# Kernel tuning notes

Measured on AMD Instinct MI355X. Metric: run time of the kernel, lower is better.

The kernel has to match this reference:

```python
import jax, jax.numpy as jnp
import numpy as np

B_SZ, L, H, P, G, N, CS = 2, 2048, 32, 64, 1, 128, 256


def _i8(k, shape):
    return jax.random.randint(k, shape, -127, 128, dtype=jnp.int32).astype(jnp.int8)


def setup_inputs() -> dict:
    key = jax.random.key(0)
    k = jax.random.split(key, 7)
    return {
        "x": _i8(k[0], (B_SZ, L, H, P)),          # quantized int8 activations
        "dt": _i8(k[1], (B_SZ, L, H)),
        "B": _i8(k[2], (B_SZ, L, G, N)),
        "C": _i8(k[3], (B_SZ, L, G, N)),
        "q_A_log": _i8(k[4], (H,)),               # int8 quantized A_log
        "q_D": _i8(k[5], (H,)),                   # int8 quantized D (D_has_hdim=False)
        "dt_bias": jax.random.normal(k[6], (H,), jnp.float32) * 0.1,
        "A_log_scale": jnp.float32(0.02),
        "D_scale": jnp.float32(0.01),
        "dt_scale": jnp.float32(0.03),
        "x_scale": jnp.float32(0.05),
        "B_scale": jnp.float32(0.05),
        "C_scale": jnp.float32(0.05),
    }


def _chunk_scan(x, dt, B, C, q_A_log, q_D, dt_bias,
                A_log_scale, D_scale, dt_scale, x_scale, B_scale, C_scale):
    f32 = jnp.float32
    b, l, h, p = x.shape
    g, n = B.shape[2], B.shape[3]
    cs = CS
    nc = l // cs

    # --- inline dequantization (per-tensor scales, nhead/ndim groups == 0) ---
    xf = x.astype(f32) * x_scale                       # (b, l, h, p)
    dtf = jax.nn.softplus(dt.astype(f32) * dt_scale + dt_bias)   # (b, l, h), dt_limit=(0, inf)
    A = -jnp.exp(q_A_log.astype(f32) * A_log_scale)    # (h,)
    Bf = B.astype(f32) * B_scale                       # (b, l, g, n)
    Cf = C.astype(f32) * C_scale

    # --- chunk the sequence ---
    xc = xf.reshape(b, nc, cs, h, p)
    dtc = dtf.reshape(b, nc, cs, h)
    Bc = Bf.reshape(b, nc, cs, g, n)
    Cc = Cf.reshape(b, nc, cs, g, n)
    rep = h // g
    Bh = jnp.repeat(Bc, rep, axis=3)                   # (b, nc, cs, h, n)
    Ch = jnp.repeat(Cc, rep, axis=3)

    dA = dtc * A                                       # (b, nc, cs, h), <= 0
    cum = jnp.cumsum(dA, axis=2)                       # cumulative log-decay within chunk

    # --- per-chunk states: sum_s exp(cum[-1]-cum[s]) * dt[s] * B[s] (x) x[s] ---
    decay_states = jnp.exp(cum[:, :, -1:, :] - cum)    # (b, nc, cs, h)
    states = jnp.einsum('bzlhn,bzlh,bzlhp->bzhpn', Bh, dtc * decay_states, xc)

    # --- inter-chunk recurrence (sequential scan over chunks) ---
    chunk_decay = jnp.exp(cum[:, :, -1, :])            # (b, nc, h)

    def step(carry, inp):
        s_c, d_c = inp                                 # (b, h, p, n), (b, h)
        new = d_c[:, :, None, None] * carry + s_c
        return new, carry                              # emit state entering this chunk

    states_t = jnp.moveaxis(states, 1, 0)              # (nc, b, h, p, n)
    decay_t = jnp.moveaxis(chunk_decay, 1, 0)          # (nc, b, h)
    final_state, prev_states = jax.lax.scan(
        step, jnp.zeros((b, h, p, n), f32), (states_t, decay_t))
    prev_states = jnp.moveaxis(prev_states, 0, 1)      # (b, nc, h, p, n)

    # --- inter-chunk output: C[l] . state_in * exp(cum[l]) ---
    y_inter = jnp.einsum('bzlhn,bzhpn,bzlh->bzlhp', Ch, prev_states, jnp.exp(cum))

    # --- intra-chunk output: causal (C.B) attention with decay weights ---
    cumT = jnp.moveaxis(cum, 3, 2)                     # (b, nc, h, cs)
    diff = cumT[..., :, None] - cumT[..., None, :]     # (b, nc, h, cs, cs): cum[l]-cum[s]
    mask = jnp.tril(jnp.ones((cs, cs), bool))
    decay_m = jnp.exp(jnp.where(mask, diff, -jnp.inf)) # zero above diagonal, no overflow
    scores = (jnp.einsum('bzlhn,bzshn->bzhls', Ch, Bh)
              * decay_m
              * jnp.moveaxis(dtc, 3, 2)[..., None, :])
    y_intra = jnp.einsum('bzhls,bzshp->bzlhp', scores, xc)

    # --- skip connection D * x (per-head D) ---
    Df = q_D.astype(f32) * D_scale                     # (h,)
    y = (y_intra + y_inter).reshape(b, l, h, p) + xf * Df[None, None, :, None]
    return y


def reference(x, dt, B, C, q_A_log, q_D, dt_bias,
              A_log_scale, D_scale, dt_scale, x_scale, B_scale, C_scale):
    return _chunk_scan(x, dt, B, C, q_A_log, q_D, dt_bias,
                       A_log_scale, D_scale, dt_scale, x_scale, B_scale, C_scale)
```

## Files before the change

kernel.cpp:

```cpp
#include <hip/hip_runtime.h>
#include <math.h>

#define BB 2
#define LSEQ 2048
#define H 32
#define PDIM 64
#define NDIM 128
#define CS 256
#define NC 8

typedef _Float16 half8 __attribute__((ext_vector_type(8)));
typedef _Float16 half4 __attribute__((ext_vector_type(4)));
typedef float floatx4 __attribute__((ext_vector_type(4)));


__device__ __forceinline__ int dot4i8(int a, int b, int c) {
#if __has_builtin(__builtin_amdgcn_sdot4)
    return __builtin_amdgcn_sdot4(a, b, c, false);
#else
    c += ((a << 24) >> 24) * ((b << 24) >> 24);
    c += ((a << 16) >> 24) * ((b << 16) >> 24);
    c += ((a << 8) >> 24) * ((b << 8) >> 24);
    c += (a >> 24) * (b >> 24);
    return c;
#endif
}

__global__ __launch_bounds__(256) void kA(
    const int* __restrict__ Bm, const int* __restrict__ Cm,
    const float* __restrict__ Bs_p, const float* __restrict__ Cs_p,
    float* __restrict__ CBt, _Float16* __restrict__ Bt16T, _Float16* __restrict__ C16T)
{
    __shared__ int Bi[64][33];
    __shared__ int Ci[64][33];
    int t = threadIdx.x;
    int r = blockIdx.x % 26;
    int zz = blockIdx.x / 26;
    int z = zz & 7, b = zz >> 3;
    int bz = b * NC + z;
    if (r < 10) {
        const int LT[10] = {0,1,1,2,2,2,3,3,3,3};
        const int ST[10] = {0,0,1,0,1,2,0,1,2,3};
        int l0 = LT[r] * 64, s0 = ST[r] * 64;
        const int* Bp = Bm + (size_t)(b * LSEQ + z * CS + s0) * NDIM;
        const int* Cp = Cm + (size_t)(b * LSEQ + z * CS + l0) * NDIM;
        for (int i = t; i < 64 * 32; i += 256) {
            int rr = i >> 5, k = i & 31;
            const int* sb = Bp + rr * NDIM + k * 4;
            const int* sc = Cp + rr * NDIM + k * 4;
            Bi[rr][k] = (sb[0] & 255) | ((sb[1] & 255) << 8) | ((sb[2] & 255) << 16) | ((sb[3] & 255) << 24);
            Ci[rr][k] = (sc[0] & 255) | ((sc[1] & 255) << 8) | ((sc[2] & 255) << 16) | ((sc[3] & 255) << 24);
        }
        __syncthreads();
        float cbscale = (*Bs_p) * (*Cs_p);
        int ll = t & 63, lg = t >> 6;
        int acc[16];
#pragma unroll
        for (int i = 0; i < 16; ++i) acc[i] = 0;
        for (int k = 0; k < 32; ++k) {
            int cw = Ci[ll][k];
#pragma unroll
            for (int si = 0; si < 16; ++si)
                acc[si] = dot4i8(cw, Bi[lg * 16 + si][k], acc[si]);
        }
        int l = l0 + ll;
        int l16 = l >> 4, lm = l & 15;
        int sb8 = (s0 + lg * 16) >> 3;
        float* bp = CBt + ((size_t)(bz * 16 + l16) * 32 + sb8) * 128 + lm * 8;
#pragma unroll
        for (int g = 0; g < 2; ++g) {
            floatx4 v0, v1;
#pragma unroll
            for (int i = 0; i < 4; ++i) {
                v0[i] = (float)acc[g * 8 + i] * cbscale;
                v1[i] = (float)acc[g * 8 + 4 + i] * cbscale;
            }
            *(floatx4*)(bp + g * 128) = v0;
            *(floatx4*)(bp + g * 128 + 4) = v1;
        }
    } else {
        int slice = r - 10;
        {
            int lm = t >> 4, n8 = t & 15;
            const int* cp = Cm + (size_t)(b * LSEQ + z * CS + slice * 16 + lm) * NDIM + n8 * 8;
            int4 c0 = *(const int4*)cp;
            int4 c1 = *(const int4*)(cp + 4);
            half8 v;
            v[0] = (_Float16)(float)c0.x; v[1] = (_Float16)(float)c0.y;
            v[2] = (_Float16)(float)c0.z; v[3] = (_Float16)(float)c0.w;
            v[4] = (_Float16)(float)c1.x; v[5] = (_Float16)(float)c1.y;
            v[6] = (_Float16)(float)c1.z; v[7] = (_Float16)(float)c1.w;
            *(half8*)(C16T + ((size_t)(bz * 16 + slice) * 16 + n8) * 128 + lm * 8) = v;
        }
        {
            int nm = t & 15, s8l = t >> 4;
            int n16 = slice & 7, s8 = (slice >> 3) * 16 + s8l;
            const int* bp = Bm + (size_t)(b * LSEQ + z * CS + s8 * 8) * NDIM + n16 * 16 + nm;
            half8 v;
#pragma unroll
            for (int j = 0; j < 8; ++j) v[j] = (_Float16)(float)bp[(size_t)j * NDIM];
            *(half8*)(Bt16T + ((size_t)(bz * 8 + n16) * 32 + s8) * 128 + nm * 8) = v;
        }
    }
}

#define XC_PITCH 132
__global__ __launch_bounds__(256) void k013(
    const int* __restrict__ dt, const int* __restrict__ qA, const float* __restrict__ dt_bias,
    const float* __restrict__ A_scale_p, const float* __restrict__ dt_scale_p,
    const int* __restrict__ xq, const float* __restrict__ xs_p, const float* __restrict__ Bs_p,
    const _Float16* __restrict__ Bt16T,
    float* __restrict__ cum, float* __restrict__ cdecay,
    _Float16* __restrict__ xTdtT, signed char* __restrict__ x8,
    float* __restrict__ states)
{
    __shared__ float cumS[CS];
    __shared__ float cA[CS], cB[CS];
    __shared__ float wsum[4];
    __shared__ _Float16 xcS[2 * 32 * XC_PITCH];
    int t = threadIdx.x;
    int half = blockIdx.x & 1;
    int h = (blockIdx.x >> 1) & 31, z = (blockIdx.x >> 6) & 7, b = blockIdx.x >> 9;
    int bz = b * NC + z, bzh = bz * H + h;
    int lane6 = t & 63, w = t >> 6;

    float A = -__expf((float)qA[h] * (*A_scale_p));
    float raw = (float)dt[(size_t)(b * LSEQ + z * CS + t) * H + h];
    float xin = raw * (*dt_scale_p) + dt_bias[h];
    float sp = (xin > 20.f) ? xin : log1pf(__expf(xin));
    float v = sp * A;
#pragma unroll
    for (int off = 1; off < 64; off <<= 1) {
        float u = __shfl_up(v, off, 64);
        if (lane6 >= off) v += u;
    }
    if (lane6 == 63) wsum[w] = v;
    __syncthreads();
    float add = 0.f;
    for (int wv = 0; wv < w; ++wv) add += wsum[wv];
    float cumv = v + add;
    float cl = wsum[0] + wsum[1] + wsum[2] + wsum[3];
    float xs = *xs_p;
    if (half == 0) {
        cum[bzh * CS + t] = cumv;
        if (t == 0) cdecay[bzh] = __expf(cl);
    }
    cumS[t] = cumv;
    cA[t] = sp * xs;
    cB[t] = sp * __expf(cl - cumv) * xs * (*Bs_p);
    __syncthreads();

    int s8 = t & 31, pq = t >> 5;
    const int* xb = xq + ((size_t)(b * LSEQ + z * CS) * H + h) * PDIM + half * 32 + pq * 4;
    signed char* x8b = x8 + ((size_t)(b * LSEQ + z * CS) * H + h) * PDIM + half * 32 + pq * 4;
    {
        half8 va[4], vc[4];
#pragma unroll
        for (int j = 0; j < 8; ++j) {
            int s = s8 * 8 + j;
            int4 w4 = *(const int4*)(xb + (size_t)s * (H * PDIM));
            float a = cA[s], c = cB[s];
            signed char pk[4];
#define CVT(PL, V) { float xv = (float)(V); va[PL][j] = (_Float16)(xv * a); vc[PL][j] = (_Float16)(xv * c); pk[PL] = (signed char)(V); }
            CVT(0, w4.x) CVT(1, w4.y) CVT(2, w4.z) CVT(3, w4.w)
#undef CVT
            *(int*)pk;
            *(int*)(x8b + (size_t)s * (H * PDIM)) = *(int*)pk;
        }
#pragma unroll
        for (int pl = 0; pl < 4; ++pl) {
            int ploc = pq * 4 + pl;
            int p16l = ploc >> 4, pm = ploc & 15;
            *(half8*)(xTdtT + ((size_t)(bzh * 4 + half * 2 + p16l) * 32 + s8) * 128 + pm * 8) = va[pl];
            *(half8*)(xcS + (p16l * 32 + s8) * XC_PITCH + pm * 8) = vc[pl];
        }
    }
    __syncthreads();

    int m = lane6 & 15, q = lane6 >> 4;
    int p16l = w & 1, ntb = (w >> 1) * 4;
    const _Float16* abase = xcS + (p16l * 32) * XC_PITCH + m * 8;
    const _Float16* bbase = Bt16T + ((size_t)(bz * 8 + ntb) * 32) * 128 + m * 8;
    floatx4 acc[4] = {};
    for (int kk = 0; kk < 8; ++kk) {
        if (cl - cumS[kk * 32 + 31] < -30.f) continue;
        int s8k = kk * 4 + q;
        half8 a = *(const half8*)(abase + s8k * XC_PITCH);
#pragma unroll
        for (int i = 0; i < 4; ++i) {
            half8 bf = *(const half8*)(bbase + ((size_t)i * 32 + s8k) * 128);
            acc[i] = __builtin_amdgcn_mfma_f32_16x16x32_f16(a, bf, acc[i], 0, 0, 0);
        }
    }
    int p16 = half * 2 + p16l;
    float* sb = states + (size_t)bzh * (PDIM * NDIM);
#pragma unroll
    for (int i = 0; i < 4; ++i)
#pragma unroll
        for (int rr = 0; rr < 4; ++rr)
            sb[(size_t)(p16 * 16 + q * 4 + rr) * NDIM + (ntb + i) * 16 + m] = acc[i][rr];
}

__global__ __launch_bounds__(256) void k4_scan(
    const float* __restrict__ cdecay, const float* __restrict__ states,
    _Float16* __restrict__ statesHT)
{
    int idx = blockIdx.x * 256 + threadIdx.x;
    int n4 = (idx & 31) * 4, p = (idx >> 5) & 63, h = (idx >> 11) & 31, b = idx >> 16;
    int soff = p * 128 + n4;
    int toff = ((p >> 4) * 16 + (n4 >> 3)) * 128 + (p & 15) * 8 + (n4 & 7);
    floatx4 carry = {};
    for (int z = 0; z < NC; ++z) {
        int bzh = (b * NC + z) * H + h;
        floatx4 v = *(const floatx4*)(states + (size_t)bzh * 8192 + soff);
        float d = cdecay[bzh];
        half4 o;
#pragma unroll
        for (int i = 0; i < 4; ++i) o[i] = (_Float16)(carry[i] * 0.0625f);
        *(half4*)(statesHT + (size_t)bzh * 8192 + toff) = o;
#pragma unroll
        for (int i = 0; i < 4; ++i) carry[i] = d * carry[i] + v[i];
    }
}

__global__ __launch_bounds__(256) void k56(
    const signed char* __restrict__ x8, const int* __restrict__ qD,
    const float* __restrict__ cum, const float* __restrict__ CBt,
    const _Float16* __restrict__ xTdtT, const _Float16* __restrict__ C16T,
    const _Float16* __restrict__ statesHT,
    const float* __restrict__ Cs_p, const float* __restrict__ xs_p, const float* __restrict__ Ds_p,
    float* __restrict__ out)
{
    __shared__ float cumL[CS];
    __shared__ float ep[128][65];
    int t = threadIdx.x;
    int parity = blockIdx.x & 1;
    int h = (blockIdx.x >> 1) & 31, z = (blockIdx.x >> 6) & 7, b = blockIdx.x >> 9;
    int bz = b * NC + z, bzh = bz * H + h;
    cumL[t] = cum[bzh * CS + t];
    __syncthreads();
    int w = t >> 6, lane = t & 63, m = lane & 15, q = lane >> 4;
    int l16a[2] = {parity + 2 * w, parity + 2 * (7 - w)};
    floatx4 acc[2][4] = {};

    const _Float16* shb = statesHT + (size_t)bzh * 8192 + m * 8;
    const _Float16* cbase = C16T + (size_t)bz * 16 * 16 * 128 + m * 8;
    bool interact[2];
#pragma unroll
    for (int j = 0; j < 2; ++j) interact[j] = (cumL[l16a[j] * 16] > -80.f);
    for (int kk = 0; kk < 4; ++kk) {
        int n8 = kk * 4 + q;
        half8 bf[4];
#pragma unroll
        for (int pt = 0; pt < 4; ++pt)
            bf[pt] = *(const half8*)(shb + (pt * 16 + n8) * 128);
#pragma unroll
        for (int j = 0; j < 2; ++j) {
            if (!interact[j]) continue;
            half8 ha = *(const half8*)(cbase + ((size_t)l16a[j] * 16 + n8) * 128);
#pragma unroll
            for (int pt = 0; pt < 4; ++pt)
                acc[j][pt] = __builtin_amdgcn_mfma_f32_16x16x32_f16(ha, bf[pt], acc[j][pt], 0, 0, 0);
        }
    }
    float Cs16 = (*Cs_p) * 16.0f;
#pragma unroll
    for (int j = 0; j < 2; ++j)
#pragma unroll
        for (int r = 0; r < 4; ++r) {
            float e = __expf(cumL[l16a[j] * 16 + q * 4 + r]) * Cs16;
#pragma unroll
            for (int pt = 0; pt < 4; ++pt) acc[j][pt][r] *= e;
        }

    const float* cbtb = CBt + (size_t)bz * 16 * 32 * 128 + m * 8;
    const _Float16* xb = xTdtT + (size_t)bzh * 4 * 32 * 128 + m * 8;
    for (int kk = 0; kk < 8; ++kk) {
        bool ex[2];
#pragma unroll
        for (int j = 0; j < 2; ++j)
            ex[j] = (2 * kk <= l16a[j]) && (cumL[l16a[j] * 16] - cumL[kk * 32 + 31] >= -30.f);
        if (!ex[0] && !ex[1]) continue;
        int s8 = kk * 4 + q;
        half8 bf[4];
#pragma unroll
        for (int pt = 0; pt < 4; ++pt)
            bf[pt] = *(const half8*)(xb + ((size_t)pt * 32 + s8) * 128);
#pragma unroll
        for (int j = 0; j < 2; ++j) {
            if (!ex[j]) continue;
            int l16 = l16a[j];
            int lA = l16 * 16 + m;
            float cum_l = cumL[lA];
            const float* cp = cbtb + ((size_t)l16 * 32 + s8) * 128;
            floatx4 c0 = *(const floatx4*)cp;
            floatx4 c1 = *(const floatx4*)(cp + 4);
            half8 a;
#pragma unroll
            for (int jj = 0; jj < 8; ++jj) {
                int s = kk * 32 + q * 8 + jj;
                float cb = (jj < 4) ? c0[jj] : c1[jj - 4];
                float wv = cb * __expf(cum_l - cumL[s]);
                a[jj] = (_Float16)((s <= lA) ? wv : 0.f);
            }
#pragma unroll
            for (int pt = 0; pt < 4; ++pt)
                acc[j][pt] = __builtin_amdgcn_mfma_f32_16x16x32_f16(a, bf[pt], acc[j][pt], 0, 0, 0);
        }
    }

    float xsDf = (*xs_p) * ((float)qD[h] * (*Ds_p));
    __syncthreads();
#pragma unroll
    for (int j = 0; j < 2; ++j) {
        int kidx = (j == 0) ? w : 7 - w;
        int lbase = kidx * 16 + q * 4;
#pragma unroll
        for (int r = 0; r < 4; ++r)
#pragma unroll
            for (int pt = 0; pt < 4; ++pt)
                ep[lbase + r][pt * 16 + m] = acc[j][pt][r];
    }
    __syncthreads();
    int lloc = t >> 1;
    int kidx = lloc >> 4, row = lloc & 15;
    int l = (parity + 2 * kidx) * 16 + row;
    size_t go = ((size_t)(b * LSEQ + z * CS + l) * H + h) * PDIM + (t & 1) * 32;
    const float* er = &ep[lloc][(t & 1) * 32];
    const signed char* xp8 = x8 + go;
#pragma unroll
    for (int it = 0; it < 8; ++it) {
        int xw = *(const int*)(xp8 + it * 4);
        floatx4 vv;
        vv[0] = er[it * 4 + 0] + (float)((xw << 24) >> 24) * xsDf;
        vv[1] = er[it * 4 + 1] + (float)((xw << 16) >> 24) * xsDf;
        vv[2] = er[it * 4 + 2] + (float)((xw << 8) >> 24) * xsDf;
        vv[3] = er[it * 4 + 3] + (float)(xw >> 24) * xsDf;
        *(floatx4*)(out + go + it * 4) = vv;
    }
}

extern "C" void kernel_launch(void* const* d_in, const int* in_sizes, int n_in,
                              void* d_out, int out_size, void* d_ws, size_t ws_size,
                              hipStream_t stream)
{
    const int* xq = (const int*)d_in[0];
    const int* dt = (const int*)d_in[1];
    const int* Bm = (const int*)d_in[2];
    const int* Cm = (const int*)d_in[3];
    const int* qA = (const int*)d_in[4];
    const int* qD = (const int*)d_in[5];
    const float* dt_bias = (const float*)d_in[6];
    const float* A_scale = (const float*)d_in[7];
    const float* D_scale = (const float*)d_in[8];
    const float* dt_scale = (const float*)d_in[9];
    const float* x_scale = (const float*)d_in[10];
    const float* B_scale = (const float*)d_in[11];
    const float* C_scale = (const float*)d_in[12];
    float* out = (float*)d_out;

    char* ws = (char*)d_ws;
    float* cum          = (float*)(ws);
    float* cdecay       = (float*)(ws + 524288);
    float* CBt          = (float*)(ws + 526336);
    float* states       = (float*)(ws + 4720640);
    _Float16* xTdtT     = (_Float16*)(ws + 21497856);
    _Float16* statesHT  = (_Float16*)(ws + 38275072);
    _Float16* Bt16T     = (_Float16*)(ws + 46663680);
    _Float16* C16T      = (_Float16*)(ws + 47712256);
    signed char* x8     = (signed char*)(ws + 48760832);

    kA<<<dim3(416), dim3(256), 0, stream>>>(Bm, Cm, B_scale, C_scale, CBt, Bt16T, C16T);
    k013<<<dim3(1024), dim3(256), 0, stream>>>(dt, qA, dt_bias, A_scale, dt_scale,
                                               xq, x_scale, B_scale, Bt16T,
                                               cum, cdecay, xTdtT, x8, states);
    k4_scan<<<dim3(512), dim3(256), 0, stream>>>(cdecay, states, statesHT);
    k56<<<dim3(1024), dim3(256), 0, stream>>>(x8, qD, cum, CBt, xTdtT, C16T, statesHT,
                                              C_scale, x_scale, D_scale, out);
}
```

Baseline: 169.3 us.

## Store CB and chunk states in fp16 and split k56 blocks by P-half

```diff
diff --git a/kernel.cpp b/kernel.cpp
--- a/kernel.cpp
+++ b/kernel.cpp
@@ -29,7 +29,7 @@
 __global__ __launch_bounds__(256) void kA(
     const int* __restrict__ Bm, const int* __restrict__ Cm,
     const float* __restrict__ Bs_p, const float* __restrict__ Cs_p,
-    float* __restrict__ CBt, _Float16* __restrict__ Bt16T, _Float16* __restrict__ C16T)
+    _Float16* __restrict__ CBh, _Float16* __restrict__ Bt16T, _Float16* __restrict__ C16T)
 {
     __shared__ int Bi[64][33];
     __shared__ int Ci[64][33];
@@ -66,17 +66,13 @@
         int l = l0 + ll;
         int l16 = l >> 4, lm = l & 15;
         int sb8 = (s0 + lg * 16) >> 3;
-        float* bp = CBt + ((size_t)(bz * 16 + l16) * 32 + sb8) * 128 + lm * 8;
+        _Float16* bp = CBh + ((size_t)(bz * 16 + l16) * 32 + sb8) * 128 + lm * 8;
 #pragma unroll
         for (int g = 0; g < 2; ++g) {
-            floatx4 v0, v1;
-#pragma unroll
-            for (int i = 0; i < 4; ++i) {
-                v0[i] = (float)acc[g * 8 + i] * cbscale;
-                v1[i] = (float)acc[g * 8 + 4 + i] * cbscale;
-            }
-            *(floatx4*)(bp + g * 128) = v0;
-            *(floatx4*)(bp + g * 128 + 4) = v1;
+            half8 v;
+#pragma unroll
+            for (int i = 0; i < 8; ++i) v[i] = (_Float16)((float)acc[g * 8 + i] * cbscale);
+            *(half8*)(bp + g * 128) = v;
         }
     } else {
         int slice = r - 10;
@@ -112,7 +108,7 @@
     const _Float16* __restrict__ Bt16T,
     float* __restrict__ cum, float* __restrict__ cdecay,
     _Float16* __restrict__ xTdtT, signed char* __restrict__ x8,
-    float* __restrict__ states)
+    _Float16* __restrict__ statesF16)
 {
     __shared__ float cumS[CS];
     __shared__ float cA[CS], cB[CS];
@@ -142,7 +138,7 @@
     float cl = wsum[0] + wsum[1] + wsum[2] + wsum[3];
     float xs = *xs_p;
     if (half == 0) {
-        cum[bzh * CS + t] = cumv;
+        cum[(size_t)bzh * CS + t] = cumv;
         if (t == 0) cdecay[bzh] = __expf(cl);
     }
     cumS[t] = cumv;
@@ -164,7 +160,6 @@
 #define CVT(PL, V) { float xv = (float)(V); va[PL][j] = (_Float16)(xv * a); vc[PL][j] = (_Float16)(xv * c); pk[PL] = (signed char)(V); }
             CVT(0, w4.x) CVT(1, w4.y) CVT(2, w4.z) CVT(3, w4.w)
 #undef CVT
-            *(int*)pk;
             *(int*)(x8b + (size_t)s * (H * PDIM)) = *(int*)pk;
         }
 #pragma unroll
@@ -193,118 +188,113 @@
         }
     }
     int p16 = half * 2 + p16l;
-    float* sb = states + (size_t)bzh * (PDIM * NDIM);
+    _Float16* sb = statesF16 + (size_t)bzh * 8192;
 #pragma unroll
     for (int i = 0; i < 4; ++i)
 #pragma unroll
         for (int rr = 0; rr < 4; ++rr)
-            sb[(size_t)(p16 * 16 + q * 4 + rr) * NDIM + (ntb + i) * 16 + m] = acc[i][rr];
+            sb[(size_t)(p16 * 16 + (ntb + i) * 2 + (m >> 3)) * 128 + (q * 4 + rr) * 8 + (m & 7)] =
+                (_Float16)(acc[i][rr] * 0.0625f);
 }
 
 __global__ __launch_bounds__(256) void k4_scan(
-    const float* __restrict__ cdecay, const float* __restrict__ states,
+    const float* __restrict__ cdecay, const _Float16* __restrict__ statesF16,
     _Float16* __restrict__ statesHT)
 {
     int idx = blockIdx.x * 256 + threadIdx.x;
-    int n4 = (idx & 31) * 4, p = (idx >> 5) & 63, h = (idx >> 11) & 31, b = idx >> 16;
-    int soff = p * 128 + n4;
-    int toff = ((p >> 4) * 16 + (n4 >> 3)) * 128 + (p & 15) * 8 + (n4 & 7);
+    int off4 = (idx & 2047) * 4;
+    int h = (idx >> 11) & 31, b = idx >> 16;
     floatx4 carry = {};
     for (int z = 0; z < NC; ++z) {
         int bzh = (b * NC + z) * H + h;
-        floatx4 v = *(const floatx4*)(states + (size_t)bzh * 8192 + soff);
+        half4 v4 = *(const half4*)(statesF16 + (size_t)bzh * 8192 + off4);
         float d = cdecay[bzh];
         half4 o;
 #pragma unroll
-        for (int i = 0; i < 4; ++i) o[i] = (_Float16)(carry[i] * 0.0625f);
-        *(half4*)(statesHT + (size_t)bzh * 8192 + toff) = o;
-#pragma unroll
-        for (int i = 0; i < 4; ++i) carry[i] = d * carry[i] + v[i];
+        for (int i = 0; i < 4; ++i) o[i] = (_Float16)carry[i];
+        *(half4*)(statesHT + (size_t)bzh * 8192 + off4) = o;
+#pragma unroll
+        for (int i = 0; i < 4; ++i) carry[i] = d * carry[i] + (float)v4[i];
     }
 }
 
 __global__ __launch_bounds__(256) void k56(
     const signed char* __restrict__ x8, const int* __restrict__ qD,
-    const float* __restrict__ cum, const float* __restrict__ CBt,
+    const float* __restrict__ cum, const _Float16* __restrict__ CBh,
     const _Float16* __restrict__ xTdtT, const _Float16* __restrict__ C16T,
     const _Float16* __restrict__ statesHT,
     const float* __restrict__ Cs_p, const float* __restrict__ xs_p, const float* __restrict__ Ds_p,
     float* __restrict__ out)
 {
     __shared__ float cumL[CS];
-    __shared__ float ep[128][65];
+    __shared__ float ep[128][33];
     int t = threadIdx.x;
-    int parity = blockIdx.x & 1;
+    int ph = blockIdx.x & 1;
     int h = (blockIdx.x >> 1) & 31, z = (blockIdx.x >> 6) & 7, b = blockIdx.x >> 9;
     int bz = b * NC + z, bzh = bz * H + h;
-    cumL[t] = cum[bzh * CS + t];
+    cumL[t] = cum[(size_t)bzh * CS + t];
     __syncthreads();
     int w = t >> 6, lane = t & 63, m = lane & 15, q = lane >> 4;
-    int l16a[2] = {parity + 2 * w, parity + 2 * (7 - w)};
-    floatx4 acc[2][4] = {};
+    floatx4 acc[4][2] = {};
 
     const _Float16* shb = statesHT + (size_t)bzh * 8192 + m * 8;
     const _Float16* cbase = C16T + (size_t)bz * 16 * 16 * 128 + m * 8;
-    bool interact[2];
-#pragma unroll
-    for (int j = 0; j < 2; ++j) interact[j] = (cumL[l16a[j] * 16] > -80.f);
+    bool interact[4];
+#pragma unroll
+    for (int j = 0; j < 4; ++j) interact[j] = (cumL[(4 * j + w) * 16] > -80.f);
     for (int kk = 0; kk < 4; ++kk) {
         int n8 = kk * 4 + q;
-        half8 bf[4];
-#pragma unroll
-        for (int pt = 0; pt < 4; ++pt)
-            bf[pt] = *(const half8*)(shb + (pt * 16 + n8) * 128);
-#pragma unroll
-        for (int j = 0; j < 2; ++j) {
+        half8 bf[2];
+#pragma unroll
+        for (int pt = 0; pt < 2; ++pt)
+            bf[pt] = *(const half8*)(shb + ((ph * 2 + pt) * 16 + n8) * 128);
+#pragma unroll
+        for (int j = 0; j < 4; ++j) {
             if (!interact[j]) continue;
-            half8 ha = *(const half8*)(cbase + ((size_t)l16a[j] * 16 + n8) * 128);
-#pragma unroll
-            for (int pt = 0; pt < 4; ++pt)
+            half8 ha = *(const half8*)(cbase + ((size_t)(4 * j + w) * 16 + n8) * 128);
+#pragma unroll
+            for (int pt = 0; pt < 2; ++pt)
                 acc[j][pt] = __builtin_amdgcn_mfma_f32_16x16x32_f16(ha, bf[pt], acc[j][pt], 0, 0, 0);
         }
     }
     float Cs16 = (*Cs_p) * 16.0f;
 #pragma unroll
-    for (int j = 0; j < 2; ++j)
+    for (int j = 0; j < 4; ++j)
 #pragma unroll
         for (int r = 0; r < 4; ++r) {
-            float e = __expf(cumL[l16a[j] * 16 + q * 4 + r]) * Cs16;
-#pragma unroll
-            for (int pt = 0; pt < 4; ++pt) acc[j][pt][r] *= e;
-        }
-
-    const float* cbtb = CBt + (size_t)bz * 16 * 32 * 128 + m * 8;
+            float e = __expf(cumL[(4 * j + w) * 16 + q * 4 + r]) * Cs16;
+#pragma unroll
+            for (int pt = 0; pt < 2; ++pt) acc[j][pt][r] *= e;
+        }
+
+    const _Float16* cbtb = CBh + (size_t)bz * 16 * 32 * 128 + m * 8;
     const _Float16* xb = xTdtT + (size_t)bzh * 4 * 32 * 128 + m * 8;
     for (int kk = 0; kk < 8; ++kk) {
-        bool ex[2];
-#pragma unroll
-        for (int j = 0; j < 2; ++j)
-            ex[j] = (2 * kk <= l16a[j]) && (cumL[l16a[j] * 16] - cumL[kk * 32 + 31] >= -30.f);
-        if (!ex[0] && !ex[1]) continue;
+        int jmin = (2 * kk - w + 3) >> 2;
+        if (jmin < 0) jmin = 0;
+        if (jmin > 3) continue;
         int s8 = kk * 4 + q;
-        half8 bf[4];
-#pragma unroll
-        for (int pt = 0; pt < 4; ++pt)
-            bf[pt] = *(const half8*)(xb + ((size_t)pt * 32 + s8) * 128);
-#pragma unroll
-        for (int j = 0; j < 2; ++j) {
-            if (!ex[j]) continue;
-            int l16 = l16a[j];
+        half8 bf[2];
+#pragma unroll
+        for (int pt = 0; pt < 2; ++pt)
+            bf[pt] = *(const half8*)(xb + ((size_t)((ph * 2 + pt) * 32 + s8)) * 128);
+#pragma unroll
+        for (int j = 0; j < 4; ++j) {
+            if (j < jmin) continue;
+            int l16 = 4 * j + w;
+            if (cumL[l16 * 16] - cumL[kk * 32 + 31] < -30.f) continue;
             int lA = l16 * 16 + m;
             float cum_l = cumL[lA];
-            const float* cp = cbtb + ((size_t)l16 * 32 + s8) * 128;
-            floatx4 c0 = *(const floatx4*)cp;
-            floatx4 c1 = *(const floatx4*)(cp + 4);
+            half8 cb8 = *(const half8*)(cbtb + ((size_t)l16 * 32 + s8) * 128);
             half8 a;
 #pragma unroll
             for (int jj = 0; jj < 8; ++jj) {
                 int s = kk * 32 + q * 8 + jj;
-                float cb = (jj < 4) ? c0[jj] : c1[jj - 4];
-                float wv = cb * __expf(cum_l - cumL[s]);
+                float wv = (float)cb8[jj] * __expf(cum_l - cumL[s]);
                 a[jj] = (_Float16)((s <= lA) ? wv : 0.f);
             }
 #pragma unroll
-            for (int pt = 0; pt < 4; ++pt)
+            for (int pt = 0; pt < 2; ++pt)
                 acc[j][pt] = __builtin_amdgcn_mfma_f32_16x16x32_f16(a, bf[pt], acc[j][pt], 0, 0, 0);
         }
     }
@@ -312,31 +302,34 @@
     float xsDf = (*xs_p) * ((float)qD[h] * (*Ds_p));
     __syncthreads();
 #pragma unroll
-    for (int j = 0; j < 2; ++j) {
-        int kidx = (j == 0) ? w : 7 - w;
-        int lbase = kidx * 16 + q * 4;
-#pragma unroll
-        for (int r = 0; r < 4; ++r)
-#pragma unroll
-            for (int pt = 0; pt < 4; ++pt)
-                ep[lbase + r][pt * 16 + m] = acc[j][pt][r];
-    }
-    __syncthreads();
-    int lloc = t >> 1;
-    int kidx = lloc >> 4, row = lloc & 15;
-    int l = (parity + 2 * kidx) * 16 + row;
-    size_t go = ((size_t)(b * LSEQ + z * CS + l) * H + h) * PDIM + (t & 1) * 32;
-    const float* er = &ep[lloc][(t & 1) * 32];
-    const signed char* xp8 = x8 + go;
-#pragma unroll
-    for (int it = 0; it < 8; ++it) {
-        int xw = *(const int*)(xp8 + it * 4);
-        floatx4 vv;
-        vv[0] = er[it * 4 + 0] + (float)((xw << 24) >> 24) * xsDf;
-        vv[1] = er[it * 4 + 1] + (float)((xw << 16) >> 24) * xsDf;
-        vv[2] = er[it * 4 + 2] + (float)((xw << 8) >> 24) * xsDf;
-        vv[3] = er[it * 4 + 3] + (float)(xw >> 24) * xsDf;
-        *(floatx4*)(out + go + it * 4) = vv;
+    for (int pass = 0; pass < 2; ++pass) {
+#pragma unroll
+        for (int jj = 0; jj < 2; ++jj) {
+            int j = pass * 2 + jj;
+            int lbase = (((4 * j + w) * 16) & 127) + q * 4;
+#pragma unroll
+            for (int r = 0; r < 4; ++r)
+#pragma unroll
+                for (int pt = 0; pt < 2; ++pt)
+                    ep[lbase + r][pt * 16 + m] = acc[j][pt][r];
+        }
+        __syncthreads();
+        int lloc = t >> 1;
+        int l = pass * 128 + lloc;
+        size_t go = ((size_t)(b * LSEQ + z * CS + l) * H + h) * PDIM + ph * 32 + (t & 1) * 16;
+        const float* er = &ep[lloc][(t & 1) * 16];
+        const signed char* xp8 = x8 + go;
+#pragma unroll
+        for (int it = 0; it < 4; ++it) {
+            int xw = *(const int*)(xp8 + it * 4);
+            floatx4 vv;
+            vv[0] = er[it * 4 + 0] + (float)((xw << 24) >> 24) * xsDf;
+            vv[1] = er[it * 4 + 1] + (float)((xw << 16) >> 24) * xsDf;
+            vv[2] = er[it * 4 + 2] + (float)((xw << 8) >> 24) * xsDf;
+            vv[3] = er[it * 4 + 3] + (float)(xw >> 24) * xsDf;
+            *(floatx4*)(out + go + it * 4) = vv;
+        }
+        __syncthreads();
     }
 }
 
@@ -360,21 +353,21 @@
     float* out = (float*)d_out;
 
     char* ws = (char*)d_ws;
-    float* cum          = (float*)(ws);
-    float* cdecay       = (float*)(ws + 524288);
-    float* CBt          = (float*)(ws + 526336);
-    float* states       = (float*)(ws + 4720640);
-    _Float16* xTdtT     = (_Float16*)(ws + 21497856);
-    _Float16* statesHT  = (_Float16*)(ws + 38275072);
-    _Float16* Bt16T     = (_Float16*)(ws + 46663680);
-    _Float16* C16T      = (_Float16*)(ws + 47712256);
-    signed char* x8     = (signed char*)(ws + 48760832);
-
-    kA<<<dim3(416), dim3(256), 0, stream>>>(Bm, Cm, B_scale, C_scale, CBt, Bt16T, C16T);
+    float* cum           = (float*)(ws);
+    float* cdecay        = (float*)(ws + 524288);
+    _Float16* CBh        = (_Float16*)(ws + 526336);
+    _Float16* statesF16  = (_Float16*)(ws + 2623488);
+    _Float16* statesHT   = (_Float16*)(ws + 11012096);
+    _Float16* xTdtT      = (_Float16*)(ws + 19400704);
+    _Float16* Bt16T      = (_Float16*)(ws + 36177920);
+    _Float16* C16T       = (_Float16*)(ws + 37226496);
+    signed char* x8      = (signed char*)(ws + 38275072);
+
+    kA<<<dim3(416), dim3(256), 0, stream>>>(Bm, Cm, B_scale, C_scale, CBh, Bt16T, C16T);
     k013<<<dim3(1024), dim3(256), 0, stream>>>(dt, qA, dt_bias, A_scale, dt_scale,
                                                xq, x_scale, B_scale, Bt16T,
-                                               cum, cdecay, xTdtT, x8, states);
-    k4_scan<<<dim3(512), dim3(256), 0, stream>>>(cdecay, states, statesHT);
-    k56<<<dim3(1024), dim3(256), 0, stream>>>(x8, qD, cum, CBt, xTdtT, C16T, statesHT,
+                                               cum, cdecay, xTdtT, x8, statesF16);
+    k4_scan<<<dim3(512), dim3(256), 0, stream>>>(cdecay, statesF16, statesHT);
+    k56<<<dim3(1024), dim3(256), 0, stream>>>(x8, qD, cum, CBh, xTdtT, C16T, statesHT,
                                               C_scale, x_scale, D_scale, out);
 }
```

Measured after the change: 169.0 us. No clear change (-0.2%).
